# Kernel optimization log

Hardware: AMD Instinct MI355X
Metric: run time of the kernel (lower is better)

Reference implementation:

```python
import jax, jax.numpy as jnp
import numpy as np

N = 100_000   # nodes (patches)
E = 500_000   # directed edges (kNN, k=5)
F_IN, NHID, GDIM, NCLS = 512, 128, 32, 3
RATIO = 0.2

def _k(n):
    return int(np.ceil(RATIO * n))

K1, K2, K3 = _k(N), _k(_k(N)), _k(_k(_k(N)))


def setup_inputs() -> dict:
    key = jax.random.key(0)
    ks = jax.random.split(key, 20)
    def w(k, shape):
        fan_in = shape[0]
        return jax.random.normal(k, shape, jnp.float32) / np.sqrt(fan_in)
    return {
        "x": jax.random.normal(ks[0], (N, F_IN), jnp.float32),
        "edge_index": jax.random.randint(ks[1], (2, E), 0, N, jnp.int32),
        # SAGEConv1 (lin_l on aggregated msgs w/ bias, lin_r on root w/o bias)
        "w1l": w(ks[2], (F_IN, NHID)), "b1l": jnp.zeros((NHID,), jnp.float32),
        "w1r": w(ks[3], (F_IN, NHID)),
        # SAGPooling1 score GNN = GCNConv(nhid, 1)
        "g1w": w(ks[4], (NHID, 1)), "g1b": jnp.zeros((1,), jnp.float32),
        "w2l": w(ks[5], (NHID, NHID)), "b2l": jnp.zeros((NHID,), jnp.float32),
        "w2r": w(ks[6], (NHID, NHID)),
        "g2w": w(ks[7], (NHID, 1)), "g2b": jnp.zeros((1,), jnp.float32),
        "w3l": w(ks[8], (NHID, NHID)), "b3l": jnp.zeros((NHID,), jnp.float32),
        "w3r": w(ks[9], (NHID, NHID)),
        "g3w": w(ks[10], (NHID, 1)), "g3b": jnp.zeros((1,), jnp.float32),
        "lw1": w(ks[11], (2 * NHID, NHID)), "lb1": jnp.zeros((NHID,), jnp.float32),
        "lw2": w(ks[12], (NHID, GDIM)), "lb2": jnp.zeros((GDIM,), jnp.float32),
        "lw3": w(ks[13], (GDIM, NCLS)), "lb3": jnp.zeros((NCLS,), jnp.float32),
    }


def sage_conv(x, src, dst, ev, Wl, bl, Wr, n):
    """PyG SAGEConv: lin_l(mean_{j->i} x_j) + lin_r(x_i); ev is float edge-valid mask."""
    msg = x[src] * ev[:, None]                      # [E, F] gather
    agg = jax.ops.segment_sum(msg, dst, num_segments=n)
    cnt = jax.ops.segment_sum(ev, dst, num_segments=n)
    mean = agg / jnp.maximum(cnt, 1.0)[:, None]
    return mean @ Wl + bl + x @ Wr


def gcn_score(x, src, dst, ev, W, b, n):
    """GCNConv(nhid,1) with self-loops and symmetric norm -> per-node score [n]."""
    xw = x @ W                                       # [n, 1]
    deg = jax.ops.segment_sum(ev, dst, num_segments=n) + 1.0  # self-loop
    dis = jax.lax.rsqrt(deg)
    norm = dis[src] * dis[dst] * ev                  # [E]
    agg = jax.ops.segment_sum(xw[src] * norm[:, None], dst, num_segments=n)
    agg = agg + xw * (dis * dis)[:, None]            # self-loop term
    return (agg + b)[:, 0]


def sag_pool(x, src, dst, ev, W, b, n, k):
    """SAGPooling: top-k by GCN score, x' = x[perm] * tanh(score[perm]); relabel/mask edges."""
    score = gcn_score(x, src, dst, ev, W, b, n)
    topv, perm = jax.lax.top_k(score, k)
    xk = x[perm] * jnp.tanh(topv)[:, None]
    rank = jnp.full((n,), -1, jnp.int32).at[perm].set(jnp.arange(k, dtype=jnp.int32))
    ns, nd = rank[src], rank[dst]
    nev = ev * ((ns >= 0) & (nd >= 0)).astype(x.dtype)
    return xk, jnp.maximum(ns, 0), jnp.maximum(nd, 0), nev


def reference(x, edge_index, w1l, b1l, w1r, g1w, g1b, w2l, b2l, w2r, g2w, g2b,
              w3l, b3l, w3r, g3w, g3b, lw1, lb1, lw2, lb2, lw3, lb3):
    src, dst = edge_index[0], edge_index[1]
    ev = jnp.ones((src.shape[0],), x.dtype)

    h = jax.nn.relu(sage_conv(x, src, dst, ev, w1l, b1l, w1r, N))
    h, src, dst, ev = sag_pool(h, src, dst, ev, g1w, g1b, N, K1)
    x1 = jnp.concatenate([h.max(axis=0), h.mean(axis=0)])[None]   # [1, 2*nhid]

    h = jax.nn.relu(sage_conv(h, src, dst, ev, w2l, b2l, w2r, K1))
    h, src, dst, ev = sag_pool(h, src, dst, ev, g2w, g2b, K1, K2)
    x2 = jnp.concatenate([h.max(axis=0), h.mean(axis=0)])[None]

    h = jax.nn.relu(sage_conv(h, src, dst, ev, w3l, b3l, w3r, K2))
    h, src, dst, ev = sag_pool(h, src, dst, ev, g3w, g3b, K2, K3)
    x3 = jnp.concatenate([h.max(axis=0), h.mean(axis=0)])[None]

    g = x1 + x2 + x3
    g = jax.nn.relu(g @ lw1 + lb1)          # dropout is identity in eval
    features = jax.nn.relu(g @ lw2 + lb2)   # [1, grph_dim]
    out = features @ lw3 + lb3              # [1, num_classes], act=None
    return features, out
```

## Files before the change

kernel.cpp:

```cpp
#include <hip/hip_runtime.h>
#include <hip/hip_bf16.h>
#include <cstdint>
#include <cstddef>

#define N_NODES 100000
#define N_EDGES 500000
#define F_IN    512
#define NHID    128
#define KP1     20000
#define KP2     4000
#define KP3     800
#define GDIM    32
#define NCLS    3
#define HISTB   128
#define RELB    768

typedef __attribute__((ext_vector_type(8))) short bf16x8;
typedef __attribute__((ext_vector_type(4))) float f32x4;

static __device__ __forceinline__ unsigned enc_f(float f) {
  unsigned u = __float_as_uint(f);
  return (u & 0x80000000u) ? ~u : (u | 0x80000000u);
}
static __device__ __forceinline__ float dec_f(unsigned u) {
  unsigned v = (u & 0x80000000u) ? (u & 0x7FFFFFFFu) : ~u;
  return __uint_as_float(v);
}
static __device__ __forceinline__ unsigned short f2bf(float f) {
  unsigned u = __float_as_uint(f);
  return (unsigned short)((u + 0x7FFFu + ((u >> 16) & 1u)) >> 16);
}
static __device__ __forceinline__ unsigned pk2(float a, float b) {
  return (unsigned)f2bf(a) | ((unsigned)f2bf(b) << 16);
}
static __device__ __forceinline__ float bf2f(unsigned short v) {
  return __uint_as_float(((unsigned)v) << 16);
}

static __device__ __forceinline__ void hist_tail(int hb, int t, int nthreads,
                                                 const int* __restrict__ dst,
                                                 const int* __restrict__ ev,
                                                 int* __restrict__ cnt) {
  for (int e = hb * nthreads + t; e < N_EDGES; e += HISTB * nthreads) {
    if (ev && !ev[e]) continue;
    atomicAdd(cnt + dst[e], 1);
  }
}

__global__ __launch_bounds__(256) void wt_prep(const float* __restrict__ w1l,
                                               const float* __restrict__ w1r,
                                               const float* __restrict__ w2l,
                                               const float* __restrict__ w2r,
                                               const float* __restrict__ w3l,
                                               const float* __restrict__ w3r,
                                               unsigned short* __restrict__ Wt,
                                               unsigned short* __restrict__ Wt2,
                                               unsigned short* __restrict__ Wt3,
                                               int* __restrict__ cnt0,
                                               unsigned* __restrict__ hist) {
  __shared__ unsigned short T[128][130];
  int blk = blockIdx.x;
  int t = threadIdx.x;
  if (blk == 0) hist[t] = 0u;
  for (int i = blk * 256 + t; i < N_NODES; i += (int)gridDim.x * 256) cnt0[i] = 0;

  const float* W;
  unsigned short* Wo;
  int mat, k0, KW;
  if (blk < 8) {
    mat = blk >> 2; k0 = (blk & 3) * 128; KW = 512;
    W = mat ? w1r : w1l; Wo = Wt;
  } else if (blk < 10) {
    mat = blk - 8; k0 = 0; KW = 128;
    W = mat ? w2r : w2l; Wo = Wt2;
  } else {
    mat = blk - 10; k0 = 0; KW = 128;
    W = mat ? w3r : w3l; Wo = Wt3;
  }
  for (int q = 0; q < 64; ++q) {
    int idx = q * 256 + t;
    int r = idx >> 7, c = idx & 127;
    T[r][c] = f2bf(W[(size_t)(k0 + r) * 128 + c]);
  }
  __syncthreads();
  int nn = t & 127;
  int kc = (t >> 7) * 64;
  for (int j8 = 0; j8 < 8; ++j8) {
    uint4 w;
    int kb = kc + j8 * 8;
    w.x = (unsigned)T[kb + 0][nn] | ((unsigned)T[kb + 1][nn] << 16);
    w.y = (unsigned)T[kb + 2][nn] | ((unsigned)T[kb + 3][nn] << 16);
    w.z = (unsigned)T[kb + 4][nn] | ((unsigned)T[kb + 5][nn] << 16);
    w.w = (unsigned)T[kb + 6][nn] | ((unsigned)T[kb + 7][nn] << 16);
    *reinterpret_cast<uint4*>(Wo + ((size_t)(mat * 128 + nn) * KW + k0 + kb)) = w;
  }
}

__global__ __launch_bounds__(512) void gemm_mfma(const float* __restrict__ A,
                                                 const unsigned short* __restrict__ Wt,
                                                 unsigned short* __restrict__ O1b,
                                                 float* __restrict__ O2, int n, int K, int nbA,
                                                 const int* __restrict__ edst,
                                                 const int* __restrict__ eev,
                                                 int* __restrict__ cnt) {
  const int t = threadIdx.x;
  if ((int)blockIdx.x >= nbA) {
    hist_tail(blockIdx.x - nbA, t, 512, edst, eev, cnt);
    return;
  }
  __shared__ unsigned short Alds[128 * 64];
  const int wave = t >> 6;
  const int lane = t & 63;
  const int wr = wave >> 2;
  const int wc = wave & 3;
  const int l15 = lane & 15, l4 = lane >> 4;
  const int bm = blockIdx.x * 128;
  f32x4 zero = {0.f, 0.f, 0.f, 0.f};
  f32x4 acc[4][4];
#pragma unroll
  for (int i = 0; i < 4; ++i)
#pragma unroll
    for (int j = 0; j < 4; ++j) acc[i][j] = zero;

  const int sr = t >> 2;
  const int skc = (t & 3) * 16;
  const int sgr = bm + sr;
  const float* ap = A + (size_t)sgr * K + skc;
  const unsigned sbase = sr * 128 + skc * 2;
  const unsigned ssw = (sr & 7) << 4;

  for (int k0 = 0; k0 < K; k0 += 64) {
    __syncthreads();
    {
      float4 v0, v1, v2, v3;
      if (sgr < n) {
        v0 = *reinterpret_cast<const float4*>(ap + k0);
        v1 = *reinterpret_cast<const float4*>(ap + k0 + 4);
        v2 = *reinterpret_cast<const float4*>(ap + k0 + 8);
        v3 = *reinterpret_cast<const float4*>(ap + k0 + 12);
      } else {
        v0 = v1 = v2 = v3 = make_float4(0.f, 0.f, 0.f, 0.f);
      }
      uint4 w0, w1;
      w0.x = pk2(v0.x, v0.y); w0.y = pk2(v0.z, v0.w);
      w0.z = pk2(v1.x, v1.y); w0.w = pk2(v1.z, v1.w);
      w1.x = pk2(v2.x, v2.y); w1.y = pk2(v2.z, v2.w);
      w1.z = pk2(v3.x, v3.y); w1.w = pk2(v3.z, v3.w);
      *reinterpret_cast<uint4*>((char*)Alds + (sbase ^ ssw)) = w0;
      *reinterpret_cast<uint4*>((char*)Alds + ((sbase + 16) ^ ssw)) = w1;
    }
    __syncthreads();
#pragma unroll
    for (int kk = 0; kk < 2; ++kk) {
      bf16x8 af[4], bfr[4];
#pragma unroll
      for (int fr = 0; fr < 4; ++fr) {
        int row = wr * 64 + fr * 16 + l15;
        unsigned ba = (unsigned)(row * 128 + kk * 64 + l4 * 16) ^ ((unsigned)(row & 7) << 4);
        af[fr] = *reinterpret_cast<const bf16x8*>((const char*)Alds + ba);
      }
#pragma unroll
      for (int fn = 0; fn < 4; ++fn) {
        int col = wc * 64 + fn * 16 + l15;
        bfr[fn] = *reinterpret_cast<const bf16x8*>(Wt + ((size_t)col * K + k0 + kk * 32 + l4 * 8));
      }
#pragma unroll
      for (int fr = 0; fr < 4; ++fr)
#pragma unroll
        for (int fn = 0; fn < 4; ++fn)
          acc[fr][fn] = __builtin_amdgcn_mfma_f32_16x16x32_bf16(af[fr], bfr[fn], acc[fr][fn], 0, 0, 0);
    }
  }

#pragma unroll
  for (int fr = 0; fr < 4; ++fr) {
#pragma unroll
    for (int fn = 0; fn < 4; ++fn) {
      int colg = wc * 64 + fn * 16 + l15;
      int col = colg & 127;
      int row0 = bm + wr * 64 + fr * 16 + l4 * 4;
#pragma unroll
      for (int r2 = 0; r2 < 4; ++r2) {
        int gr = row0 + r2;
        if (gr < n) {
          if (colg < 128) O1b[(size_t)gr * 128 + col] = f2bf(acc[fr][fn][r2]);
          else            O2 [(size_t)gr * 128 + col] = acc[fr][fn][r2];
        }
      }
    }
  }
}

__global__ void scan1(const int* __restrict__ cnt, int n,
                      int* __restrict__ incl, int* __restrict__ bsum) {
  __shared__ int sh[256];
  int t = threadIdx.x, i = blockIdx.x * 256 + t;
  int v = (i < n) ? cnt[i] : 0;
  sh[t] = v; __syncthreads();
  for (int o = 1; o < 256; o <<= 1) {
    int a = (t >= o) ? sh[t - o] : 0;
    __syncthreads(); sh[t] += a; __syncthreads();
  }
  if (i < n) incl[i] = sh[t];
  if (t == 255) bsum[blockIdx.x] = sh[255];
}

__global__ void scan2(int* __restrict__ bsum, int nb) {
  __shared__ int sh[512];
  int t = threadIdx.x;
  int v = (t < nb) ? bsum[t] : 0;
  sh[t] = v; __syncthreads();
  for (int o = 1; o < 512; o <<= 1) {
    int a = (t >= o) ? sh[t - o] : 0;
    __syncthreads(); sh[t] += a; __syncthreads();
  }
  if (t < nb) bsum[t] = sh[t] - v;
}

__global__ void scan3(const int* __restrict__ cnt, const int* __restrict__ incl,
                      const int* __restrict__ bsum, int n,
                      int* __restrict__ rowstart, int* __restrict__ ptr,
                      int* __restrict__ cnt_next, int n_next) {
  int i = blockIdx.x * 256 + threadIdx.x;
  if (i < n_next) cnt_next[i] = 0;
  if (i >= n) return;
  int excl = incl[i] - cnt[i] + bsum[blockIdx.x];
  rowstart[i] = excl; ptr[i] = excl;
  if (i == n - 1) rowstart[n] = excl + cnt[i];
}

__global__ __launch_bounds__(1024) void csr_scan_one(const int* __restrict__ cnt, int n,
                                                     int* __restrict__ rowstart,
                                                     int* __restrict__ ptr,
                                                     int* __restrict__ cnt_next, int n_next) {
  __shared__ int sg[1024];
  const int t = threadIdx.x;
  for (int i = t; i < n_next; i += 1024) cnt_next[i] = 0;
  const int chunk = (n + 1023) >> 10;
  const int i0 = t * chunk;
  const int i1 = (i0 + chunk < n) ? i0 + chunk : n;
  int c = 0;
  for (int i = i0; i < i1; ++i) c += cnt[i];
  sg[t] = c;
  __syncthreads();
  for (int o = 1; o < 1024; o <<= 1) {
    int a = (t >= o) ? sg[t - o] : 0;
    __syncthreads();
    sg[t] += a;
    __syncthreads();
  }
  int excl = sg[t] - c;
  for (int i = i0; i < i1; ++i) {
    rowstart[i] = excl; ptr[i] = excl;
    excl += cnt[i];
  }
  if (t == 1023) rowstart[n] = sg[1023];
}

__global__ void scatter_csr(const int* __restrict__ src, const int* __restrict__ dst,
                            const int* __restrict__ ev, int* __restrict__ ptr,
                            int* __restrict__ csr_src) {
  int e = blockIdx.x * 256 + threadIdx.x;
  if (e >= N_EDGES) return;
  if (ev && !ev[e]) return;
  int p = atomicAdd(ptr + dst[e], 1);
  csr_src[p] = src[e];
}

__global__ void segsort(const int* __restrict__ rowstart, int* __restrict__ csr, int n) {
  int i = blockIdx.x * 256 + threadIdx.x;
  if (i >= n) return;
  int b = rowstart[i], e = rowstart[i + 1];
  for (int j = b + 1; j < e; ++j) {
    int v = csr[j], k = j - 1;
    while (k >= b && csr[k] > v) { csr[k + 1] = csr[k]; --k; }
    csr[k + 1] = v;
  }
}

__global__ void agg_fin(const unsigned short* __restrict__ X1b, const int* __restrict__ rowstart,
                        const int* __restrict__ csr, const float* __restrict__ bias,
                        const float* __restrict__ gw,
                        float* __restrict__ G, float* __restrict__ xw, int n) {
  int wid = (blockIdx.x * 256 + threadIdx.x) >> 6;
  if (wid >= n) return;
  int lane = threadIdx.x & 63;
  int b = rowstart[wid], e = rowstart[wid + 1];
  float sx = 0.f, sy = 0.f;
  int p = b;
  for (; p + 1 < e; p += 2) {
    int s0 = csr[p], s1 = csr[p + 1];
    unsigned v0 = *reinterpret_cast<const unsigned*>(X1b + (size_t)s0 * 128 + lane * 2);
    unsigned v1 = *reinterpret_cast<const unsigned*>(X1b + (size_t)s1 * 128 + lane * 2);
    sx += bf2f((unsigned short)(v0 & 0xFFFFu));
    sy += bf2f((unsigned short)(v0 >> 16));
    sx += bf2f((unsigned short)(v1 & 0xFFFFu));
    sy += bf2f((unsigned short)(v1 >> 16));
  }
  if (p < e) {
    int s0 = csr[p];
    unsigned v0 = *reinterpret_cast<const unsigned*>(X1b + (size_t)s0 * 128 + lane * 2);
    sx += bf2f((unsigned short)(v0 & 0xFFFFu));
    sy += bf2f((unsigned short)(v0 >> 16));
  }
  int c = e - b; if (c < 1) c = 1;
  float inv = 1.f / (float)c;
  float2 bi = *reinterpret_cast<const float2*>(bias + lane * 2);
  float2 g  = *reinterpret_cast<const float2*>(G + (size_t)wid * 128 + lane * 2);
  float2 o = make_float2(fmaxf(sx * inv + bi.x + g.x, 0.f),
                         fmaxf(sy * inv + bi.y + g.y, 0.f));
  *reinterpret_cast<float2*>(G + (size_t)wid * 128 + lane * 2) = o;
  float2 gwv = *reinterpret_cast<const float2*>(gw + lane * 2);
  float s = o.x * gwv.x + o.y * gwv.y;
  for (int off = 32; off; off >>= 1) s += __shfl_down(s, off);
  if (lane == 0) xw[wid] = s;
}

__global__ void gcn_score_csr(const float* __restrict__ xw, const int* __restrict__ rowstart,
                              const int* __restrict__ csr, const int* __restrict__ cnt,
                              const float* __restrict__ gb,
                              float* __restrict__ score, unsigned* __restrict__ keys, int n,
                              unsigned* __restrict__ state, int kout) {
  int i = blockIdx.x * 256 + threadIdx.x;
  if (i == 0) { state[0] = 0u; state[1] = (unsigned)kout; }
  if (i >= n) return;
  int b = rowstart[i], e = rowstart[i + 1];
  float di = rsqrtf((float)(e - b) + 1.f);
  float s = 0.f;
  int p = b;
  for (; p + 1 < e; p += 2) {
    int s0 = csr[p], s1 = csr[p + 1];
    float x0 = xw[s0], x1 = xw[s1];
    float c0 = (float)cnt[s0], c1 = (float)cnt[s1];
    s += x0 * rsqrtf(c0 + 1.f);
    s += x1 * rsqrtf(c1 + 1.f);
  }
  if (p < e) {
    int s0 = csr[p];
    s += xw[s0] * rsqrtf((float)cnt[s0] + 1.f);
  }
  float sc = s * di + xw[i] * di * di + gb[0];
  score[i] = sc;
  keys[i] = enc_f(sc);
}

__global__ void topk_hist(const unsigned* __restrict__ keys, int n,
                          const unsigned* __restrict__ state, unsigned mask, int shift,
                          unsigned* __restrict__ hist) {
  __shared__ unsigned h[256];
  int t = threadIdx.x;
  h[t] = 0u;
  __syncthreads();
  unsigned pref = state[0];
  for (int i = blockIdx.x * 256 + t; i < n; i += gridDim.x * 256) {
    unsigned k = keys[i];
    if ((k & mask) == pref) atomicAdd(&h[(k >> shift) & 0xFFu], 1u);
  }
  __syncthreads();
  unsigned hv = h[t];
  if (hv) atomicAdd(&hist[t], hv);
}

__global__ void topk_pick(unsigned* state, unsigned* hist, int shift) {
  __shared__ unsigned h[256], a[256];
  int t = threadIdx.x;
  unsigned hv = hist[t];
  hist[t] = 0;
  h[t] = hv;
  __syncthreads();
  a[t] = h[255 - t];
  __syncthreads();
  for (int o = 1; o < 256; o <<= 1) {
    unsigned v = (t >= o) ? a[t - o] : 0u;
    __syncthreads();
    a[t] += v;
    __syncthreads();
  }
  unsigned krem = state[1];
  unsigned Sb  = a[255 - t];
  unsigned Sb1 = (t == 255) ? 0u : a[255 - (t + 1)];
  if (Sb >= krem && Sb1 < krem) {
    state[0] |= ((unsigned)t) << shift;
    state[1] = krem - Sb1;
  }
}

__global__ void scanA(const unsigned* __restrict__ keys, int n,
                      const unsigned* __restrict__ state,
                      unsigned* __restrict__ pgt, unsigned* __restrict__ peq) {
  __shared__ unsigned sg[256], se[256];
  int t = threadIdx.x;
  int i = blockIdx.x * 256 + t;
  unsigned kth = state[0];
  unsigned g = 0, e = 0;
  if (i < n) { unsigned k = keys[i]; g = (k > kth); e = (k == kth); }
  sg[t] = g; se[t] = e;
  __syncthreads();
  for (int s = 128; s; s >>= 1) {
    if (t < s) { sg[t] += sg[t + s]; se[t] += se[t + s]; }
    __syncthreads();
  }
  if (t == 0) { pgt[blockIdx.x] = sg[0]; peq[blockIdx.x] = se[0]; }
}

__global__ void scanB(unsigned* pgt, unsigned* peq, int nb,
                      unsigned* __restrict__ maxacc, float* __restrict__ sumacc) {
  __shared__ unsigned a[512], b[512];
  int t = threadIdx.x;
  if (t < 128) { maxacc[t] = 0u; sumacc[t] = 0.f; }
  unsigned og = (t < nb) ? pgt[t] : 0u;
  unsigned oe = (t < nb) ? peq[t] : 0u;
  a[t] = og; b[t] = oe;
  __syncthreads();
  for (int o = 1; o < 512; o <<= 1) {
    unsigned av = (t >= o) ? a[t - o] : 0u;
    unsigned bv = (t >= o) ? b[t - o] : 0u;
    __syncthreads();
    a[t] += av; b[t] += bv;
    __syncthreads();
  }
  if (t < nb) { pgt[t] = a[t] - og; peq[t] = b[t] - oe; }
}

__global__ void scanC(const unsigned* __restrict__ keys, int n,
                      const unsigned* __restrict__ state,
                      const unsigned* __restrict__ pgt, const unsigned* __restrict__ peq,
                      int K, int* __restrict__ rank) {
  __shared__ unsigned sg[256], se[256];
  int t = threadIdx.x;
  int i = blockIdx.x * 256 + t;
  unsigned kth = state[0], krem = state[1];
  unsigned g = 0, e = 0;
  if (i < n) { unsigned k = keys[i]; g = (k > kth); e = (k == kth); }
  sg[t] = g; se[t] = e;
  __syncthreads();
  for (int o = 1; o < 256; o <<= 1) {
    unsigned av = (t >= o) ? sg[t - o] : 0u;
    unsigned bv = (t >= o) ? se[t - o] : 0u;
    __syncthreads();
    sg[t] += av; se[t] += bv;
    __syncthreads();
  }
  if (i < n) {
    int r = -1;
    unsigned n_gt = (unsigned)K - krem;
    if (g) r = (int)(pgt[blockIdx.x] + sg[t] - 1);
    else if (e) {
      unsigned pe = peq[blockIdx.x] + se[t] - 1;
      if (pe < krem) r = (int)(n_gt + pe);
    }
    rank[i] = r;
  }
}

__global__ __launch_bounds__(1024) void select_one(const unsigned* __restrict__ keys, int n,
                                                   int K, int* __restrict__ rank,
                                                   unsigned* __restrict__ maxacc,
                                                   float* __restrict__ sumacc) {
  __shared__ unsigned h[256], a[256];
  __shared__ unsigned sg[1024], se[1024];
  __shared__ unsigned s_pref, s_krem;
  const int t = threadIdx.x;
  if (t < 128) { maxacc[t] = 0u; sumacc[t] = 0.f; }
  if (t == 0) { s_pref = 0u; s_krem = (unsigned)K; }
  __syncthreads();

#pragma unroll
  for (int p = 0; p < 4; ++p) {
    const int shift = 24 - 8 * p;
    const unsigned mask = (p == 0) ? 0u : (0xFFFFFFFFu << (shift + 8));
    if (t < 256) h[t] = 0u;
    __syncthreads();
    unsigned pref = s_pref;
    for (int i = t; i < n; i += 1024) {
      unsigned k = keys[i];
      if ((k & mask) == pref) atomicAdd(&h[(k >> shift) & 0xFFu], 1u);
    }
    __syncthreads();
    if (t < 256) a[t] = h[255 - t];
    __syncthreads();
    for (int o = 1; o < 256; o <<= 1) {
      unsigned v = (t >= o && t < 256) ? a[t - o] : 0u;
      __syncthreads();
      if (t < 256) a[t] += v;
      __syncthreads();
    }
    unsigned krem = s_krem;
    __syncthreads();
    if (t < 256) {
      unsigned Sb  = a[255 - t];
      unsigned Sb1 = (t == 255) ? 0u : a[255 - (t + 1)];
      if (Sb >= krem && Sb1 < krem) {
        s_pref |= ((unsigned)t) << shift;
        s_krem = krem - Sb1;
      }
    }
    __syncthreads();
  }

  const unsigned kth = s_pref;
  const unsigned krem = s_krem;
  const unsigned n_gt = (unsigned)K - krem;
  const int chunk = (n + 1023) >> 10;
  const int i0 = t * chunk;
  const int i1 = (i0 + chunk < n) ? i0 + chunk : n;
  unsigned cg = 0, ce = 0;
  for (int i = i0; i < i1; ++i) {
    unsigned k = keys[i];
    cg += (k > kth); ce += (k == kth);
  }
  sg[t] = cg; se[t] = ce;
  __syncthreads();
  for (int o = 1; o < 1024; o <<= 1) {
    unsigned ag = (t >= o) ? sg[t - o] : 0u;
    unsigned ae = (t >= o) ? se[t - o] : 0u;
    __syncthreads();
    sg[t] += ag; se[t] += ae;
    __syncthreads();
  }
  unsigned rg = sg[t] - cg;
  unsigned re = se[t] - ce;
  for (int i = i0; i < i1; ++i) {
    unsigned k = keys[i];
    int r = -1;
    if (k > kth) {
      r = (int)(rg++);
    } else if (k == kth) {
      unsigned pe = re++;
      if (pe < krem) r = (int)(n_gt + pe);
    }
    rank[i] = r;
  }
}

__global__ void pool_rel(const float* __restrict__ G, const float* __restrict__ score,
                         const int* __restrict__ rank, float* __restrict__ Hout, int n,
                         int nbP, int mode,
                         const int* __restrict__ ei,
                         int* __restrict__ src2, int* __restrict__ dst2,
                         int* __restrict__ ev2) {
  const int t = threadIdx.x;
  if ((int)blockIdx.x >= nbP) {
    int hb = blockIdx.x - nbP;
    if (mode == 0) {
      for (int e = hb * 256 + t; e < N_EDGES; e += RELB * 256) {
        int s = ei[e], d = ei[N_EDGES + e];
        int rs = rank[s], rd = rank[d];
        int valid = (rs >= 0) & (rd >= 0);
        src2[e] = rs > 0 ? rs : 0;
        dst2[e] = rd > 0 ? rd : 0;
        ev2[e] = valid;
      }
    } else if (mode == 1) {
      for (int e = hb * 256 + t; e < N_EDGES; e += RELB * 256) {
        if (!ev2[e]) continue;
        int s = src2[e], d = dst2[e];
        int rs = rank[s], rd = rank[d];
        int valid = (rs >= 0) & (rd >= 0);
        src2[e] = rs > 0 ? rs : 0;
        dst2[e] = rd > 0 ? rd : 0;
        ev2[e] = valid;
      }
    }
    return;
  }
  int gid = blockIdx.x * 256 + t;
  int i = gid >> 5;
  if (i >= n) return;
  int r = rank[i];
  if (r < 0) return;
  int q = gid & 31;
  float tv = tanhf(score[i]);
  float4 v = *reinterpret_cast<const float4*>(G + (size_t)i * 128 + q * 4);
  v.x *= tv; v.y *= tv; v.z *= tv; v.w *= tv;
  *reinterpret_cast<float4*>(Hout + (size_t)r * 128 + q * 4) = v;
}

__global__ void readout_reduce(const float* __restrict__ H, int k,
                               unsigned* __restrict__ maxacc, float* __restrict__ sumacc) {
  int f = threadIdx.x;
  float m = -INFINITY, s = 0.f;
  for (int r = blockIdx.x; r < k; r += gridDim.x) {
    float v = H[(size_t)r * 128 + f];
    m = fmaxf(m, v);
    s += v;
  }
  atomicMax(maxacc + f, enc_f(m));
  atomicAdd(sumacc + f, s);
}

__global__ void head_kernel(const unsigned* __restrict__ maxacc3,
                            const float* __restrict__ sumacc3,
                            const float* __restrict__ lw1, const float* __restrict__ lb1,
                            const float* __restrict__ lw2, const float* __restrict__ lb2,
                            const float* __restrict__ lw3, const float* __restrict__ lb3,
                            float* __restrict__ out) {
  __shared__ float g[256];
  __shared__ float t1[128];
  __shared__ float t2[32];
  int t = threadIdx.x;
  float v;
  if (t < 128) {
    v = dec_f(maxacc3[t]) + dec_f(maxacc3[128 + t]) + dec_f(maxacc3[256 + t]);
  } else {
    int f = t - 128;
    v = sumacc3[f] * (1.f / (float)KP1) + sumacc3[128 + f] * (1.f / (float)KP2) +
        sumacc3[256 + f] * (1.f / (float)KP3);
  }
  g[t] = v;
  __syncthreads();
  if (t < 128) {
    float s = lb1[t];
    for (int j = 0; j < 256; ++j) s += g[j] * lw1[j * 128 + t];
    t1[t] = fmaxf(s, 0.f);
  }
  __syncthreads();
  if (t < 32) {
    float s = lb2[t];
    for (int j = 0; j < 128; ++j) s += t1[j] * lw2[j * 32 + t];
    float v2 = fmaxf(s, 0.f);
    t2[t] = v2;
    out[t] = v2;
  }
  __syncthreads();
  if (t < NCLS) {
    float s = lb3[t];
    for (int j = 0; j < 32; ++j) s += t2[j] * lw3[j * 3 + t];
    out[32 + t] = s;
  }
}

extern "C" void kernel_launch(void* const* d_in, const int* in_sizes, int n_in_,
                              void* d_out, int out_size, void* d_ws, size_t ws_size,
                              hipStream_t stream) {
  (void)in_sizes; (void)n_in_; (void)out_size; (void)ws_size;
  const float* x   = (const float*)d_in[0];
  const int*   ei  = (const int*)d_in[1];
  const float* w1l = (const float*)d_in[2];
  const float* b1l = (const float*)d_in[3];
  const float* w1r = (const float*)d_in[4];
  const float* g1w = (const float*)d_in[5];
  const float* g1b = (const float*)d_in[6];
  const float* w2l = (const float*)d_in[7];
  const float* b2l = (const float*)d_in[8];
  const float* w2r = (const float*)d_in[9];
  const float* g2w = (const float*)d_in[10];
  const float* g2b = (const float*)d_in[11];
  const float* w3l = (const float*)d_in[12];
  const float* b3l = (const float*)d_in[13];
  const float* w3r = (const float*)d_in[14];
  const float* g3w = (const float*)d_in[15];
  const float* g3b = (const float*)d_in[16];
  const float* lw1 = (const float*)d_in[17];
  const float* lb1 = (const float*)d_in[18];
  const float* lw2 = (const float*)d_in[19];
  const float* lb2 = (const float*)d_in[20];
  const float* lw3 = (const float*)d_in[21];
  const float* lb3 = (const float*)d_in[22];
  float* out = (float*)d_out;

  char* base = (char*)d_ws;
  size_t off = 0;
  auto alloc = [&](size_t bytes) {
    void* p = base + off;
    off = (off + bytes + 255) & ~(size_t)255;
    return p;
  };
  unsigned short* X1b = (unsigned short*)alloc((size_t)N_NODES * 128 * 2);
  float*    G      = (float*)alloc((size_t)N_NODES * 128 * 4);
  float*    H2     = (float*)alloc((size_t)KP1 * 128 * 4);
  float*    H3     = (float*)alloc((size_t)KP2 * 128 * 4);
  float*    H4     = (float*)alloc((size_t)KP3 * 128 * 4);
  int*      cntA   = (int*)alloc((size_t)N_NODES * 4);
  int*      cntB   = (int*)alloc((size_t)KP1 * 4);
  int*      incl   = (int*)alloc((size_t)N_NODES * 4);
  int*      bsum   = (int*)alloc(512 * 4);
  int*      rowstart = (int*)alloc((size_t)(N_NODES + 1) * 4);
  int*      ptr    = (int*)alloc((size_t)N_NODES * 4);
  int*      csr    = (int*)alloc((size_t)N_EDGES * 4);
  float*    xw     = (float*)alloc((size_t)N_NODES * 4);
  float*    score  = (float*)alloc((size_t)N_NODES * 4);
  unsigned* keys   = (unsigned*)alloc((size_t)N_NODES * 4);
  int*      rank   = (int*)alloc((size_t)N_NODES * 4);
  int*      src2   = (int*)alloc((size_t)N_EDGES * 4);
  int*      dst2   = (int*)alloc((size_t)N_EDGES * 4);
  int*      ev2    = (int*)alloc((size_t)N_EDGES * 4);
  unsigned* pgt    = (unsigned*)alloc(512 * 4);
  unsigned* peq    = (unsigned*)alloc(512 * 4);
  unsigned* hist   = (unsigned*)alloc(256 * 4);
  unsigned* state  = (unsigned*)alloc(64);
  unsigned* maxacc3 = (unsigned*)alloc(3 * 128 * 4);
  float*    sumacc3 = (float*)alloc(3 * 128 * 4);
  unsigned short* Wt  = (unsigned short*)alloc((size_t)256 * 512 * 2);
  unsigned short* Wt2 = (unsigned short*)alloc((size_t)256 * 128 * 2);
  unsigned short* Wt3 = (unsigned short*)alloc((size_t)256 * 128 * 2);

  struct Layer {
    const float* H; int n; int K; int kout;
    const float *bl, *gw, *gb;
    const unsigned short* Wt;
    float* Hout;
    int* cnt;
    int* cnt_next;
    int n_next;
  };
  Layer L[3] = {
    { x,  N_NODES, F_IN, KP1, b1l, g1w, g1b, Wt,  H2, cntA, cntB, KP1 },
    { H2, KP1,     NHID, KP2, b2l, g2w, g2b, Wt2, H3, cntB, cntA, KP2 },
    { H3, KP2,     NHID, KP3, b3l, g3w, g3b, Wt3, H4, cntA, nullptr, 0 },
  };

  wt_prep<<<12, 256, 0, stream>>>(w1l, w1r, w2l, w2r, w3l, w3r, Wt, Wt2, Wt3, cntA, hist);

  for (int l = 0; l < 3; ++l) {
    const Layer& P = L[l];
    const int n = P.n;
    const int nb = (n + 255) / 256;
    const bool small = (n <= 4000);
    const int* esrc = (l == 0) ? ei            : src2;
    const int* edst = (l == 0) ? ei + N_EDGES  : dst2;
    const int* eev  = (l == 0) ? (const int*)nullptr : ev2;

    {
      int nbA = (n + 127) / 128;
      gemm_mfma<<<dim3(nbA + HISTB), 512, 0, stream>>>(P.H, P.Wt, X1b, G, n, P.K, nbA,
                                                       edst, eev, P.cnt);
    }

    if (small) {
      csr_scan_one<<<1, 1024, 0, stream>>>(P.cnt, n, rowstart, ptr, P.cnt_next, P.n_next);
    } else {
      scan1<<<nb, 256, 0, stream>>>(P.cnt, n, incl, bsum);
      scan2<<<1, 512, 0, stream>>>(bsum, nb);
      scan3<<<nb, 256, 0, stream>>>(P.cnt, incl, bsum, n, rowstart, ptr, P.cnt_next, P.n_next);
    }
    scatter_csr<<<(N_EDGES + 255) / 256, 256, 0, stream>>>(esrc, edst, eev, ptr, csr);
    segsort<<<nb, 256, 0, stream>>>(rowstart, csr, n);

    agg_fin<<<(n * 64 + 255) / 256, 256, 0, stream>>>(X1b, rowstart, csr, P.bl, P.gw, G, xw, n);

    gcn_score_csr<<<nb, 256, 0, stream>>>(xw, rowstart, csr, P.cnt, P.gb, score, keys, n,
                                          state, P.kout);

    if (small) {
      select_one<<<1, 1024, 0, stream>>>(keys, n, P.kout, rank,
                                         maxacc3 + l * 128, sumacc3 + l * 128);
    } else {
      int hb = nb < 256 ? nb : 256;
      for (int p = 0; p < 4; ++p) {
        int shift = 24 - 8 * p;
        unsigned mask = (p == 0) ? 0u : (0xFFFFFFFFu << (shift + 8));
        topk_hist<<<hb, 256, 0, stream>>>(keys, n, state, mask, shift, hist);
        topk_pick<<<1, 256, 0, stream>>>(state, hist, shift);
      }
      scanA<<<nb, 256, 0, stream>>>(keys, n, state, pgt, peq);
      scanB<<<1, 512, 0, stream>>>(pgt, peq, nb, maxacc3 + l * 128, sumacc3 + l * 128);
      scanC<<<nb, 256, 0, stream>>>(keys, n, state, pgt, peq, P.kout, rank);
    }

    int mode = (l == 0) ? 0 : (l == 1 ? 1 : 2);
    int nbP = (n * 32 + 255) / 256;
    int grid = nbP + (mode < 2 ? RELB : 0);
    pool_rel<<<grid, 256, 0, stream>>>(G, score, rank, P.Hout, n, nbP, mode,
                                       ei, src2, dst2, ev2);

    readout_reduce<<<64, 128, 0, stream>>>(P.Hout, P.kout, maxacc3 + l * 128, sumacc3 + l * 128);
  }

  head_kernel<<<1, 256, 0, stream>>>(maxacc3, sumacc3, lw1, lb1, lw2, lb2, lw3, lb3, out);
}
```

Baseline: 515.7 us.

## Store intermediate node features in bf16 and fuse readout into next GEMM launch

```diff
diff --git a/kernel.cpp b/kernel.cpp
--- a/kernel.cpp
+++ b/kernel.cpp
@@ -13,6 +13,7 @@
 #define GDIM    32
 #define NCLS    3
 #define HISTB   128
+#define RDB     64
 #define RELB    768
 
 typedef __attribute__((ext_vector_type(8))) short bf16x8;
@@ -96,19 +97,48 @@
   }
 }
 
-__global__ __launch_bounds__(512) void gemm_mfma(const float* __restrict__ A,
+__global__ __launch_bounds__(512) void gemm_mfma(const void* __restrict__ Ain, int aBf16,
                                                  const unsigned short* __restrict__ Wt,
                                                  unsigned short* __restrict__ O1b,
-                                                 float* __restrict__ O2, int n, int K, int nbA,
+                                                 unsigned short* __restrict__ Gb,
+                                                 int n, int K, int nbA,
                                                  const int* __restrict__ edst,
                                                  const int* __restrict__ eev,
-                                                 int* __restrict__ cnt) {
+                                                 int* __restrict__ cnt,
+                                                 const unsigned short* __restrict__ Hprev,
+                                                 int kprev,
+                                                 unsigned* __restrict__ maxaccP,
+                                                 float* __restrict__ sumaccP) {
+  __shared__ unsigned short Alds[128 * 64];
+  __shared__ float red[4][128];
   const int t = threadIdx.x;
+  if ((int)blockIdx.x >= nbA + HISTB) {
+    int hb = blockIdx.x - nbA - HISTB;
+    int f = t & 127, rg = t >> 7;
+    float m = -INFINITY, s = 0.f;
+    for (int r = hb * 4 + rg; r < kprev; r += RDB * 4) {
+      float v = bf2f(Hprev[(size_t)r * 128 + f]);
+      m = fmaxf(m, v); s += v;
+    }
+    red[rg][f] = m;
+    __syncthreads();
+    if (t < 128) {
+      float mm = fmaxf(fmaxf(red[0][t], red[1][t]), fmaxf(red[2][t], red[3][t]));
+      atomicMax(maxaccP + t, enc_f(mm));
+    }
+    __syncthreads();
+    red[rg][f] = s;
+    __syncthreads();
+    if (t < 128) {
+      float ss = red[0][t] + red[1][t] + red[2][t] + red[3][t];
+      atomicAdd(sumaccP + t, ss);
+    }
+    return;
+  }
   if ((int)blockIdx.x >= nbA) {
     hist_tail(blockIdx.x - nbA, t, 512, edst, eev, cnt);
     return;
   }
-  __shared__ unsigned short Alds[128 * 64];
   const int wave = t >> 6;
   const int lane = t & 63;
   const int wr = wave >> 2;
@@ -125,19 +155,28 @@
   const int sr = t >> 2;
   const int skc = (t & 3) * 16;
   const int sgr = bm + sr;
-  const float* ap = A + (size_t)sgr * K + skc;
+  const float* apf = (const float*)Ain + (size_t)sgr * K + skc;
+  const unsigned short* apb = (const unsigned short*)Ain + (size_t)sgr * K + skc;
   const unsigned sbase = sr * 128 + skc * 2;
   const unsigned ssw = (sr & 7) << 4;
 
   for (int k0 = 0; k0 < K; k0 += 64) {
     __syncthreads();
-    {
+    if (aBf16) {
+      uint4 w0 = make_uint4(0u, 0u, 0u, 0u), w1 = make_uint4(0u, 0u, 0u, 0u);
+      if (sgr < n) {
+        w0 = *reinterpret_cast<const uint4*>(apb + k0);
+        w1 = *reinterpret_cast<const uint4*>(apb + k0 + 8);
+      }
+      *reinterpret_cast<uint4*>((char*)Alds + (sbase ^ ssw)) = w0;
+      *reinterpret_cast<uint4*>((char*)Alds + ((sbase + 16) ^ ssw)) = w1;
+    } else {
       float4 v0, v1, v2, v3;
       if (sgr < n) {
-        v0 = *reinterpret_cast<const float4*>(ap + k0);
-        v1 = *reinterpret_cast<const float4*>(ap + k0 + 4);
-        v2 = *reinterpret_cast<const float4*>(ap + k0 + 8);
-        v3 = *reinterpret_cast<const float4*>(ap + k0 + 12);
+        v0 = *reinterpret_cast<const float4*>(apf + k0);
+        v1 = *reinterpret_cast<const float4*>(apf + k0 + 4);
+        v2 = *reinterpret_cast<const float4*>(apf + k0 + 8);
+        v3 = *reinterpret_cast<const float4*>(apf + k0 + 12);
       } else {
         v0 = v1 = v2 = v3 = make_float4(0.f, 0.f, 0.f, 0.f);
       }
@@ -183,8 +222,9 @@
       for (int r2 = 0; r2 < 4; ++r2) {
         int gr = row0 + r2;
         if (gr < n) {
-          if (colg < 128) O1b[(size_t)gr * 128 + col] = f2bf(acc[fr][fn][r2]);
-          else            O2 [(size_t)gr * 128 + col] = acc[fr][fn][r2];
+          unsigned short bv = f2bf(acc[fr][fn][r2]);
+          if (colg < 128) O1b[(size_t)gr * 128 + col] = bv;
+          else            Gb [(size_t)gr * 128 + col] = bv;
         }
       }
     }
@@ -281,7 +321,7 @@
 __global__ void agg_fin(const unsigned short* __restrict__ X1b, const int* __restrict__ rowstart,
                         const int* __restrict__ csr, const float* __restrict__ bias,
                         const float* __restrict__ gw,
-                        float* __restrict__ G, float* __restrict__ xw, int n) {
+                        unsigned short* __restrict__ Gb, float* __restrict__ xw, int n) {
   int wid = (blockIdx.x * 256 + threadIdx.x) >> 6;
   if (wid >= n) return;
   int lane = threadIdx.x & 63;
@@ -306,10 +346,12 @@
   int c = e - b; if (c < 1) c = 1;
   float inv = 1.f / (float)c;
   float2 bi = *reinterpret_cast<const float2*>(bias + lane * 2);
-  float2 g  = *reinterpret_cast<const float2*>(G + (size_t)wid * 128 + lane * 2);
-  float2 o = make_float2(fmaxf(sx * inv + bi.x + g.x, 0.f),
-                         fmaxf(sy * inv + bi.y + g.y, 0.f));
-  *reinterpret_cast<float2*>(G + (size_t)wid * 128 + lane * 2) = o;
+  unsigned gv = *reinterpret_cast<const unsigned*>(Gb + (size_t)wid * 128 + lane * 2);
+  float gx = bf2f((unsigned short)(gv & 0xFFFFu));
+  float gy = bf2f((unsigned short)(gv >> 16));
+  float2 o = make_float2(fmaxf(sx * inv + bi.x + gx, 0.f),
+                         fmaxf(sy * inv + bi.y + gy, 0.f));
+  *reinterpret_cast<unsigned*>(Gb + (size_t)wid * 128 + lane * 2) = pk2(o.x, o.y);
   float2 gwv = *reinterpret_cast<const float2*>(gw + lane * 2);
   float s = o.x * gwv.x + o.y * gwv.y;
   for (int off = 32; off; off >>= 1) s += __shfl_down(s, off);
@@ -533,8 +575,8 @@
   }
 }
 
-__global__ void pool_rel(const float* __restrict__ G, const float* __restrict__ score,
-                         const int* __restrict__ rank, float* __restrict__ Hout, int n,
+__global__ void pool_rel(const unsigned short* __restrict__ Gb, const float* __restrict__ score,
+                         const int* __restrict__ rank, unsigned short* __restrict__ Houtb, int n,
                          int nbP, int mode,
                          const int* __restrict__ ei,
                          int* __restrict__ src2, int* __restrict__ dst2,
@@ -571,17 +613,21 @@
   if (r < 0) return;
   int q = gid & 31;
   float tv = tanhf(score[i]);
-  float4 v = *reinterpret_cast<const float4*>(G + (size_t)i * 128 + q * 4);
-  v.x *= tv; v.y *= tv; v.z *= tv; v.w *= tv;
-  *reinterpret_cast<float4*>(Hout + (size_t)r * 128 + q * 4) = v;
-}
-
-__global__ void readout_reduce(const float* __restrict__ H, int k,
+  uint2 v = *reinterpret_cast<const uint2*>(Gb + (size_t)i * 128 + q * 4);
+  float a0 = bf2f((unsigned short)(v.x & 0xFFFFu)) * tv;
+  float a1 = bf2f((unsigned short)(v.x >> 16)) * tv;
+  float a2 = bf2f((unsigned short)(v.y & 0xFFFFu)) * tv;
+  float a3 = bf2f((unsigned short)(v.y >> 16)) * tv;
+  uint2 o = make_uint2(pk2(a0, a1), pk2(a2, a3));
+  *reinterpret_cast<uint2*>(Houtb + (size_t)r * 128 + q * 4) = o;
+}
+
+__global__ void readout_reduce(const unsigned short* __restrict__ Hb, int k,
                                unsigned* __restrict__ maxacc, float* __restrict__ sumacc) {
   int f = threadIdx.x;
   float m = -INFINITY, s = 0.f;
   for (int r = blockIdx.x; r < k; r += gridDim.x) {
-    float v = H[(size_t)r * 128 + f];
+    float v = bf2f(Hb[(size_t)r * 128 + f]);
     m = fmaxf(m, v);
     s += v;
   }
@@ -667,10 +713,10 @@
     return p;
   };
   unsigned short* X1b = (unsigned short*)alloc((size_t)N_NODES * 128 * 2);
-  float*    G      = (float*)alloc((size_t)N_NODES * 128 * 4);
-  float*    H2     = (float*)alloc((size_t)KP1 * 128 * 4);
-  float*    H3     = (float*)alloc((size_t)KP2 * 128 * 4);
-  float*    H4     = (float*)alloc((size_t)KP3 * 128 * 4);
+  unsigned short* Gb  = (unsigned short*)alloc((size_t)N_NODES * 128 * 2);
+  unsigned short* H2b = (unsigned short*)alloc((size_t)KP1 * 128 * 2);
+  unsigned short* H3b = (unsigned short*)alloc((size_t)KP2 * 128 * 2);
+  unsigned short* H4b = (unsigned short*)alloc((size_t)KP3 * 128 * 2);
   int*      cntA   = (int*)alloc((size_t)N_NODES * 4);
   int*      cntB   = (int*)alloc((size_t)KP1 * 4);
   int*      incl   = (int*)alloc((size_t)N_NODES * 4);
@@ -696,18 +742,18 @@
   unsigned short* Wt3 = (unsigned short*)alloc((size_t)256 * 128 * 2);
 
   struct Layer {
-    const float* H; int n; int K; int kout;
+    const void* H; int n; int K; int kout;
     const float *bl, *gw, *gb;
     const unsigned short* Wt;
-    float* Hout;
+    unsigned short* Hout;
     int* cnt;
     int* cnt_next;
     int n_next;
   };
   Layer L[3] = {
-    { x,  N_NODES, F_IN, KP1, b1l, g1w, g1b, Wt,  H2, cntA, cntB, KP1 },
-    { H2, KP1,     NHID, KP2, b2l, g2w, g2b, Wt2, H3, cntB, cntA, KP2 },
-    { H3, KP2,     NHID, KP3, b3l, g3w, g3b, Wt3, H4, cntA, nullptr, 0 },
+    { x,   N_NODES, F_IN, KP1, b1l, g1w, g1b, Wt,  H2b, cntA, cntB, KP1 },
+    { H2b, KP1,     NHID, KP2, b2l, g2w, g2b, Wt2, H3b, cntB, cntA, KP2 },
+    { H3b, KP2,     NHID, KP3, b3l, g3w, g3b, Wt3, H4b, cntA, nullptr, 0 },
   };
 
   wt_prep<<<12, 256, 0, stream>>>(w1l, w1r, w2l, w2r, w3l, w3r, Wt, Wt2, Wt3, cntA, hist);
@@ -723,8 +769,13 @@
 
     {
       int nbA = (n + 127) / 128;
-      gemm_mfma<<<dim3(nbA + HISTB), 512, 0, stream>>>(P.H, P.Wt, X1b, G, n, P.K, nbA,
-                                                       edst, eev, P.cnt);
+      int grid = nbA + HISTB + (l > 0 ? RDB : 0);
+      gemm_mfma<<<dim3(grid), 512, 0, stream>>>(
+          P.H, (l > 0) ? 1 : 0, P.Wt, X1b, Gb, n, P.K, nbA, edst, eev, P.cnt,
+          (l > 0) ? L[l - 1].Hout : (const unsigned short*)nullptr,
+          (l > 0) ? L[l - 1].kout : 0,
+          maxacc3 + (l > 0 ? (l - 1) : 0) * 128,
+          sumacc3 + (l > 0 ? (l - 1) : 0) * 128);
     }
 
     if (small) {
@@ -737,7 +788,7 @@
     scatter_csr<<<(N_EDGES + 255) / 256, 256, 0, stream>>>(esrc, edst, eev, ptr, csr);
     segsort<<<nb, 256, 0, stream>>>(rowstart, csr, n);
 
-    agg_fin<<<(n * 64 + 255) / 256, 256, 0, stream>>>(X1b, rowstart, csr, P.bl, P.gw, G, xw, n);
+    agg_fin<<<(n * 64 + 255) / 256, 256, 0, stream>>>(X1b, rowstart, csr, P.bl, P.gw, Gb, xw, n);
 
     gcn_score_csr<<<nb, 256, 0, stream>>>(xw, rowstart, csr, P.cnt, P.gb, score, keys, n,
                                           state, P.kout);
@@ -761,11 +812,10 @@
     int mode = (l == 0) ? 0 : (l == 1 ? 1 : 2);
     int nbP = (n * 32 + 255) / 256;
     int grid = nbP + (mode < 2 ? RELB : 0);
-    pool_rel<<<grid, 256, 0, stream>>>(G, score, rank, P.Hout, n, nbP, mode,
+    pool_rel<<<grid, 256, 0, stream>>>(Gb, score, rank, P.Hout, n, nbP, mode,
                                        ei, src2, dst2, ev2);
-
-    readout_reduce<<<64, 128, 0, stream>>>(P.Hout, P.kout, maxacc3 + l * 128, sumacc3 + l * 128);
-  }
-
+  }
+
+  readout_reduce<<<64, 128, 0, stream>>>(H4b, KP3, maxacc3 + 2 * 128, sumacc3 + 2 * 128);
   head_kernel<<<1, 256, 0, stream>>>(maxacc3, sumacc3, lw1, lb1, lw2, lb2, lw3, lb3, out);
 }
```

After: 418.7 us. 1.23x faster.
